# Kernel optimization log

Measured on AMD Instinct MI355X. Metric: run time of the kernel, lower is better.

Reference implementation:

```python
import jax, jax.numpy as jnp
import numpy as np

M, K, N = 32, 4096, 12288


def setup_inputs() -> dict:
    key = jax.random.key(0)
    k1, k2, k3, k4 = jax.random.split(key, 4)
    x = jax.random.normal(k1, (M, K), dtype=jnp.float32)
    # uint8-valued packed weight (stored as int32 for harness compatibility, values in [0,256))
    weight_u8 = jax.random.randint(k2, (K, N), 0, 256, dtype=jnp.int32)
    # per-output-channel fp16 scale and zero-point
    scale = (jax.random.uniform(k3, (N,), dtype=jnp.float32) * 0.01 + 1e-3).astype(jnp.float16)
    zero = (jax.random.uniform(k4, (N,), dtype=jnp.float32) * 255.0).astype(jnp.float16)
    return {"x": x, "weight_u8": weight_u8, "scale": scale, "zero": zero}


def reference(x, weight_u8, scale, zero):
    # QuantMatmulCustom: dequantize uint8 weight with per-channel fp16 scale/zero, then matmul.
    # w_deq[k, n] = (w_u8[k, n] - zero[n]) * scale[n]
    w_deq = (weight_u8.astype(jnp.float32) - zero.astype(jnp.float32)[None, :]) * scale.astype(jnp.float32)[None, :]
    # [M, K] @ [K, N] -> [M, N]
    return jnp.einsum('mk,kn->mn', x, w_deq)
```

## Files before the change

kernel.cpp:

```cpp
#include <hip/hip_runtime.h>

#define M_DIM 32
#define K_DIM 4096
#define N_DIM 12288
#define SPLITK 8
#define KPER  (K_DIM / SPLITK)
#define NT    (KPER / 32)
#define BLK   512
#define NPB   128

using bf16x8 = __attribute__((ext_vector_type(8))) short;
using f32x4  = __attribute__((ext_vector_type(4))) float;

typedef __attribute__((address_space(1))) const void GASV;
typedef __attribute__((address_space(3))) void LASV;

__device__ __forceinline__ short to_bf16(float f) {
    unsigned u = __float_as_uint(f);
    u += 0x7FFFu + ((u >> 16) & 1u);
    return (short)(u >> 16);
}

__device__ __forceinline__ bf16x8 pack_b(const int (&wv)[8]) {
    union { unsigned u[4]; bf16x8 v; } r;
    #pragma unroll
    for (int p = 0; p < 4; ++p) {
        unsigned a = __float_as_uint((float)wv[2 * p]);
        unsigned b = __float_as_uint((float)wv[2 * p + 1]);
        r.u[p] = __builtin_amdgcn_perm(b, a, 0x07060302);
    }
    return r.v;
}

__global__ __launch_bounds__(256) void qmm_prep(const float* __restrict__ x,
                                                short* __restrict__ frag,
                                                float* __restrict__ rowsum) {
    const int b   = blockIdx.x;
    const int tid = threadIdx.x;

    __shared__ float red[256];
    const float4* xr = (const float4*)(x + (size_t)b * K_DIM);
    float s = 0.f;
    #pragma unroll
    for (int i = 0; i < K_DIM / 4 / 256; ++i) {
        float4 v = xr[tid + 256 * i];
        s += v.x + v.y + v.z + v.w;
    }
    red[tid] = s;
    __syncthreads();
    #pragma unroll
    for (int off = 128; off > 0; off >>= 1) {
        if (tid < off) red[tid] += red[tid + off];
        __syncthreads();
    }
    if (tid == 0) rowsum[b] = red[0];

    #pragma unroll
    for (int i = 0; i < 2; ++i) {
        const int s2   = i * 256 + tid;
        const int kt   = 4 * b + (s2 >> 7);
        const int h    = (s2 >> 6) & 1;
        const int lane = s2 & 63;
        const int g    = lane >> 4;
        const int g0   = g & 1;
        const int m    = 16 * h + (lane & 15);
        const float* xp = x + (size_t)m * K_DIM + kt * 32 + 8 * g;
        float p0 = xp[0], p1 = xp[1], p2 = xp[2], p3 = xp[3];
        float p4 = xp[4], p5 = xp[5], p6 = xp[6], p7 = xp[7];
        bf16x8 v;
        v[0] = to_bf16(g0 ? p1 : p0);  v[1] = to_bf16(g0 ? p0 : p1);
        v[2] = to_bf16(g0 ? p3 : p2);  v[3] = to_bf16(g0 ? p2 : p3);
        v[4] = to_bf16(g0 ? p5 : p4);  v[5] = to_bf16(g0 ? p4 : p5);
        v[6] = to_bf16(g0 ? p7 : p6);  v[7] = to_bf16(g0 ? p6 : p7);
        *(bf16x8*)&frag[(size_t)((kt * 2 + h) * 64 + lane) * 8] = v;
    }
}

template <bool WS>
__global__ __launch_bounds__(BLK, 4) void qmm_main(const short* __restrict__ frag,
                                                   const int* __restrict__ w,
                                                   float* __restrict__ dst) {
    __shared__ int lds_b[8 * 2 * 512];

    const int tid  = threadIdx.x;
    const int lane = tid & 63;
    const int g    = lane >> 4;
    const int g0   = g & 1;
    const int c    = lane & 15;
    const int wid  = tid >> 6;
    const int k0   = blockIdx.y * KPER;
    const int n0w  = blockIdx.x * NPB + wid * 16;

    const int* gsrc[2];
    #pragma unroll
    for (int q = 0; q < 2; ++q)
        gsrc[q] = w + (size_t)(k0 + 16 * q + (lane >> 2)) * N_DIM + n0w + 4 * (lane & 3);

    int* const wbase = &lds_b[wid * 1024];

    const int vb = 4 * (128 * g + 4 * (c >> 2) + (c & 3));
    const int be = vb + 64 * g0;
    const int bo = vb + 64 * (1 - g0);

    const short* asrc = frag + ((size_t)(blockIdx.y * NT) * 1024 + lane * 8);

    f32x4 acc0 = {0.f, 0.f, 0.f, 0.f};
    f32x4 acc1 = {0.f, 0.f, 0.f, 0.f};
    bf16x8 aA0, aA1, aB0, aB1;

#define ISSUE(T) do {                                                            \
    __builtin_amdgcn_sched_barrier(0);                                           \
    __builtin_amdgcn_global_load_lds((GASV*)(gsrc[0] + (size_t)(32 * (T)) * N_DIM), \
        (LASV*)(wbase + ((T) & 1) * 512),       16, 0, 0);                       \
    __builtin_amdgcn_global_load_lds((GASV*)(gsrc[1] + (size_t)(32 * (T)) * N_DIM), \
        (LASV*)(wbase + ((T) & 1) * 512 + 256), 16, 0, 0);                       \
    if ((T) & 1) { aB0 = *(const bf16x8*)(asrc + (T) * 1024);                    \
                   aB1 = *(const bf16x8*)(asrc + (T) * 1024 + 512); }            \
    else         { aA0 = *(const bf16x8*)(asrc + (T) * 1024);                    \
                   aA1 = *(const bf16x8*)(asrc + (T) * 1024 + 512); }            \
    __builtin_amdgcn_sched_barrier(0);                                           \
} while (0)

#define WAITV(N) do { asm volatile("s_waitcnt vmcnt(" #N ")" ::: "memory");      \
    __builtin_amdgcn_sched_barrier(0); } while (0)

#define COMP(T) do {                                                             \
    char* pb = (char*)wbase + ((T) & 1) * 2048;                                  \
    int wv[8];                                                                   \
    wv[0] = *(int*)(pb + be);        wv[1] = *(int*)(pb + bo);                   \
    wv[2] = *(int*)(pb + be + 128);  wv[3] = *(int*)(pb + bo + 128);             \
    wv[4] = *(int*)(pb + be + 256);  wv[5] = *(int*)(pb + bo + 256);             \
    wv[6] = *(int*)(pb + be + 384);  wv[7] = *(int*)(pb + bo + 384);             \
    bf16x8 bfv = pack_b(wv);                                                     \
    acc0 = __builtin_amdgcn_mfma_f32_16x16x32_bf16(((T) & 1) ? aB0 : aA0, bfv, acc0, 0, 0, 0); \
    acc1 = __builtin_amdgcn_mfma_f32_16x16x32_bf16(((T) & 1) ? aB1 : aA1, bfv, acc1, 0, 0, 0); \
} while (0)

    ISSUE(0); ISSUE(1);
    WAITV(4); COMP(0);  ISSUE(2);
    WAITV(4); COMP(1);  ISSUE(3);
    WAITV(4); COMP(2);  ISSUE(4);
    WAITV(4); COMP(3);  ISSUE(5);
    WAITV(4); COMP(4);  ISSUE(6);
    WAITV(4); COMP(5);  ISSUE(7);
    WAITV(4); COMP(6);  ISSUE(8);
    WAITV(4); COMP(7);  ISSUE(9);
    WAITV(4); COMP(8);  ISSUE(10);
    WAITV(4); COMP(9);  ISSUE(11);
    WAITV(4); COMP(10); ISSUE(12);
    WAITV(4); COMP(11); ISSUE(13);
    WAITV(4); COMP(12); ISSUE(14);
    WAITV(4); COMP(13); ISSUE(15);
    WAITV(4); COMP(14);
    WAITV(0); COMP(15);

#undef ISSUE
#undef WAITV
#undef COMP

    if (WS) {
        float* pp = dst + ((size_t)blockIdx.y * M_DIM) * N_DIM + n0w + c;
        #pragma unroll
        for (int i = 0; i < 4; ++i) {
            const int r = 4 * (lane >> 4) + i;
            pp[(size_t)r * N_DIM]        = acc0[i];
            pp[(size_t)(16 + r) * N_DIM] = acc1[i];
        }
    } else {
        #pragma unroll
        for (int i = 0; i < 4; ++i) {
            const int r = 4 * (lane >> 4) + i;
            atomicAdd(&dst[(size_t)r * N_DIM + n0w + c], acc0[i]);
            atomicAdd(&dst[(size_t)(16 + r) * N_DIM + n0w + c], acc1[i]);
        }
    }
}

__global__ __launch_bounds__(256) void qmm_finalize(const float* __restrict__ part,
                                                    const float* __restrict__ rowsum,
                                                    const float* __restrict__ scale,
                                                    const float* __restrict__ zero,
                                                    float* __restrict__ out) {
    const int m  = blockIdx.y;
    const int n4 = blockIdx.x * 256 + threadIdx.x;
    const float rs = rowsum[m];
    float4 acc = make_float4(0.f, 0.f, 0.f, 0.f);
    #pragma unroll
    for (int sp = 0; sp < SPLITK; ++sp) {
        float4 p = ((const float4*)(part + ((size_t)sp * M_DIM + m) * N_DIM))[n4];
        acc.x += p.x; acc.y += p.y; acc.z += p.z; acc.w += p.w;
    }
    const float4 sc = ((const float4*)scale)[n4];
    const float4 zp = ((const float4*)zero)[n4];
    float4 o;
    o.x = sc.x * (acc.x - zp.x * rs);
    o.y = sc.y * (acc.y - zp.y * rs);
    o.z = sc.z * (acc.z - zp.z * rs);
    o.w = sc.w * (acc.w - zp.w * rs);
    ((float4*)(out + (size_t)m * N_DIM))[n4] = o;
}

__global__ __launch_bounds__(256) void qmm_zero(float* __restrict__ out) {
    int i = blockIdx.x * 256 + threadIdx.x;
    ((float4*)out)[i] = make_float4(0.f, 0.f, 0.f, 0.f);
}
__global__ __launch_bounds__(256) void qmm_scale(const float* __restrict__ x,
                                                 const float* __restrict__ scale,
                                                 const float* __restrict__ zero,
                                                 float* __restrict__ out) {
    const int m = blockIdx.y;
    __shared__ float red[256];
    float s = 0.f;
    for (int k = threadIdx.x; k < K_DIM; k += 256)
        s += x[(size_t)m * K_DIM + k];
    red[threadIdx.x] = s;
    __syncthreads();
    #pragma unroll
    for (int off = 128; off > 0; off >>= 1) {
        if (threadIdx.x < off) red[threadIdx.x] += red[threadIdx.x + off];
        __syncthreads();
    }
    const float rowsum = red[0];
    const int n = blockIdx.x * 256 + threadIdx.x;
    const float v = out[(size_t)m * N_DIM + n];
    out[(size_t)m * N_DIM + n] = scale[n] * (v - zero[n] * rowsum);
}

extern "C" void kernel_launch(void* const* d_in, const int* in_sizes, int n_in,
                              void* d_out, int out_size, void* d_ws, size_t ws_size,
                              hipStream_t stream) {
    const float* x     = (const float*)d_in[0];
    const int*   w     = (const int*)d_in[1];
    const float* scale = (const float*)d_in[2];
    const float* zero  = (const float*)d_in[3];
    float* out = (float*)d_out;

    const size_t frag_sz = (size_t)128 * 2 * 64 * 8 * sizeof(short);
    const size_t part_sz = (size_t)SPLITK * M_DIM * N_DIM * sizeof(float);
    short* fragp  = (short*)d_ws;
    float* rowsum = (float*)((char*)d_ws + frag_sz);
    float* part   = (float*)((char*)d_ws + frag_sz + 256);

    if (ws_size >= frag_sz + 256 + part_sz) {
        qmm_prep    <<<dim3(32),                 dim3(256), 0, stream>>>(x, fragp, rowsum);
        qmm_main<true><<<dim3(N_DIM / NPB, SPLITK), dim3(BLK), 0, stream>>>(fragp, w, part);
        qmm_finalize<<<dim3(N_DIM / 4 / 256, M_DIM), dim3(256), 0, stream>>>(part, rowsum, scale, zero, out);
    } else {
        qmm_prep    <<<dim3(32),                 dim3(256), 0, stream>>>(x, fragp, rowsum);
        qmm_zero    <<<dim3((M_DIM * N_DIM / 4) / 256), dim3(256), 0, stream>>>(out);
        qmm_main<false><<<dim3(N_DIM / NPB, SPLITK), dim3(BLK), 0, stream>>>(fragp, w, out);
        qmm_scale   <<<dim3(N_DIM / 256, M_DIM), dim3(256), 0, stream>>>(x, scale, zero, out);
    }
}
```

Before: 46.00 us.

## Fuse split-K reduction and dequant epilogue into main kernel via atomics

Drops the split-K partial buffer and the separate finalize kernel. The main kernel now applies the per-channel scale and the zero-point correction (only on the first K split) and atomically adds into the output. Zeroing of the output is folded into the prep kernel by enlarging its grid. This removes a kernel launch and the write and re-read of the 8-way partial buffer, at the cost of float atomics on the output, which makes the summation order nondeterministic. The fallback path is replaced by a simple non-MFMA kernel.

```diff
diff --git a/kernel.cpp b/kernel.cpp
--- a/kernel.cpp
+++ b/kernel.cpp
@@ -34,9 +34,14 @@
 
 __global__ __launch_bounds__(256) void qmm_prep(const float* __restrict__ x,
                                                 short* __restrict__ frag,
-                                                float* __restrict__ rowsum) {
-    const int b   = blockIdx.x;
+                                                float* __restrict__ rowsum,
+                                                float* __restrict__ out) {
     const int tid = threadIdx.x;
+    const int bid = blockIdx.x;
+
+    ((float4*)out)[bid * 256 + tid] = make_float4(0.f, 0.f, 0.f, 0.f);
+    if (bid >= 32) return;
+    const int b = bid;
 
     __shared__ float red[256];
     const float4* xr = (const float4*)(x + (size_t)b * K_DIM);
@@ -76,10 +81,12 @@
     }
 }
 
-template <bool WS>
 __global__ __launch_bounds__(BLK, 4) void qmm_main(const short* __restrict__ frag,
                                                    const int* __restrict__ w,
-                                                   float* __restrict__ dst) {
+                                                   const float* __restrict__ rowsum,
+                                                   const float* __restrict__ scale,
+                                                   const float* __restrict__ zero,
+                                                   float* __restrict__ out) {
     __shared__ int lds_b[8 * 2 * 512];
 
     const int tid  = threadIdx.x;
@@ -158,56 +165,57 @@
 #undef WAITV
 #undef COMP
 
-    if (WS) {
-        float* pp = dst + ((size_t)blockIdx.y * M_DIM) * N_DIM + n0w + c;
+    const float sc = scale[n0w + c];
+    float corr0[4] = {0.f, 0.f, 0.f, 0.f}, corr1[4] = {0.f, 0.f, 0.f, 0.f};
+    if (blockIdx.y == 0) {
+        const float zp = zero[n0w + c];
         #pragma unroll
         for (int i = 0; i < 4; ++i) {
             const int r = 4 * (lane >> 4) + i;
-            pp[(size_t)r * N_DIM]        = acc0[i];
-            pp[(size_t)(16 + r) * N_DIM] = acc1[i];
+            corr0[i] = zp * rowsum[r];
+            corr1[i] = zp * rowsum[16 + r];
         }
-    } else {
+    }
+    #pragma unroll
+    for (int i = 0; i < 4; ++i) {
+        const int r = 4 * (lane >> 4) + i;
+        atomicAdd(&out[(size_t)r * N_DIM + n0w + c],        sc * (acc0[i] - corr0[i]));
+        atomicAdd(&out[(size_t)(16 + r) * N_DIM + n0w + c], sc * (acc1[i] - corr1[i]));
+    }
+}
+
+__global__ __launch_bounds__(256) void qmm_zero_fb(float* __restrict__ out) {
+    int i = blockIdx.x * 256 + threadIdx.x;
+    ((float4*)out)[i] = make_float4(0.f, 0.f, 0.f, 0.f);
+}
+__global__ __launch_bounds__(256) void qmm_main_fb(const float* __restrict__ x,
+                                                   const int* __restrict__ w,
+                                                   float* __restrict__ out) {
+    const int n  = blockIdx.x * 256 + threadIdx.x;
+    const int k0 = blockIdx.y * 256;
+    float acc[M_DIM];
+    #pragma unroll
+    for (int m = 0; m < M_DIM; ++m) acc[m] = 0.f;
+    const int* wp = w + (size_t)k0 * N_DIM + n;
+    for (int kk = 0; kk < 256; kk += 4) {
+        const float w0 = (float)wp[(size_t)(kk + 0) * N_DIM];
+        const float w1 = (float)wp[(size_t)(kk + 1) * N_DIM];
+        const float w2 = (float)wp[(size_t)(kk + 2) * N_DIM];
+        const float w3 = (float)wp[(size_t)(kk + 3) * N_DIM];
         #pragma unroll
-        for (int i = 0; i < 4; ++i) {
-            const int r = 4 * (lane >> 4) + i;
-            atomicAdd(&dst[(size_t)r * N_DIM + n0w + c], acc0[i]);
-            atomicAdd(&dst[(size_t)(16 + r) * N_DIM + n0w + c], acc1[i]);
+        for (int m = 0; m < M_DIM; ++m) {
+            const float4 xv = *(const float4*)(x + (size_t)m * K_DIM + k0 + kk);
+            acc[m] = fmaf(xv.x, w0, fmaf(xv.y, w1, fmaf(xv.z, w2, fmaf(xv.w, w3, acc[m]))));
         }
     }
-}
-
-__global__ __launch_bounds__(256) void qmm_finalize(const float* __restrict__ part,
-                                                    const float* __restrict__ rowsum,
+    #pragma unroll
+    for (int m = 0; m < M_DIM; ++m)
+        atomicAdd(&out[(size_t)m * N_DIM + n], acc[m]);
+}
+__global__ __launch_bounds__(256) void qmm_scale_fb(const float* __restrict__ x,
                                                     const float* __restrict__ scale,
                                                     const float* __restrict__ zero,
                                                     float* __restrict__ out) {
-    const int m  = blockIdx.y;
-    const int n4 = blockIdx.x * 256 + threadIdx.x;
-    const float rs = rowsum[m];
-    float4 acc = make_float4(0.f, 0.f, 0.f, 0.f);
-    #pragma unroll
-    for (int sp = 0; sp < SPLITK; ++sp) {
-        float4 p = ((const float4*)(part + ((size_t)sp * M_DIM + m) * N_DIM))[n4];
-        acc.x += p.x; acc.y += p.y; acc.z += p.z; acc.w += p.w;
-    }
-    const float4 sc = ((const float4*)scale)[n4];
-    const float4 zp = ((const float4*)zero)[n4];
-    float4 o;
-    o.x = sc.x * (acc.x - zp.x * rs);
-    o.y = sc.y * (acc.y - zp.y * rs);
-    o.z = sc.z * (acc.z - zp.z * rs);
-    o.w = sc.w * (acc.w - zp.w * rs);
-    ((float4*)(out + (size_t)m * N_DIM))[n4] = o;
-}
-
-__global__ __launch_bounds__(256) void qmm_zero(float* __restrict__ out) {
-    int i = blockIdx.x * 256 + threadIdx.x;
-    ((float4*)out)[i] = make_float4(0.f, 0.f, 0.f, 0.f);
-}
-__global__ __launch_bounds__(256) void qmm_scale(const float* __restrict__ x,
-                                                 const float* __restrict__ scale,
-                                                 const float* __restrict__ zero,
-                                                 float* __restrict__ out) {
     const int m = blockIdx.y;
     __shared__ float red[256];
     float s = 0.f;
@@ -236,19 +244,15 @@
     float* out = (float*)d_out;
 
     const size_t frag_sz = (size_t)128 * 2 * 64 * 8 * sizeof(short);
-    const size_t part_sz = (size_t)SPLITK * M_DIM * N_DIM * sizeof(float);
     short* fragp  = (short*)d_ws;
     float* rowsum = (float*)((char*)d_ws + frag_sz);
-    float* part   = (float*)((char*)d_ws + frag_sz + 256);
-
-    if (ws_size >= frag_sz + 256 + part_sz) {
-        qmm_prep    <<<dim3(32),                 dim3(256), 0, stream>>>(x, fragp, rowsum);
-        qmm_main<true><<<dim3(N_DIM / NPB, SPLITK), dim3(BLK), 0, stream>>>(fragp, w, part);
-        qmm_finalize<<<dim3(N_DIM / 4 / 256, M_DIM), dim3(256), 0, stream>>>(part, rowsum, scale, zero, out);
+
+    if (ws_size >= frag_sz + 256) {
+        qmm_prep<<<dim3(M_DIM * N_DIM / 4 / 256), dim3(256), 0, stream>>>(x, fragp, rowsum, out);
+        qmm_main<<<dim3(N_DIM / NPB, SPLITK),     dim3(BLK), 0, stream>>>(fragp, w, rowsum, scale, zero, out);
     } else {
-        qmm_prep    <<<dim3(32),                 dim3(256), 0, stream>>>(x, fragp, rowsum);
-        qmm_zero    <<<dim3((M_DIM * N_DIM / 4) / 256), dim3(256), 0, stream>>>(out);
-        qmm_main<false><<<dim3(N_DIM / NPB, SPLITK), dim3(BLK), 0, stream>>>(fragp, w, out);
-        qmm_scale   <<<dim3(N_DIM / 256, M_DIM), dim3(256), 0, stream>>>(x, scale, zero, out);
-    }
-}
+        qmm_zero_fb <<<dim3(M_DIM * N_DIM / 4 / 256), dim3(256), 0, stream>>>(out);
+        qmm_main_fb <<<dim3(N_DIM / 256, 16),         dim3(256), 0, stream>>>(x, w, out);
+        qmm_scale_fb<<<dim3(N_DIM / 256, M_DIM),      dim3(256), 0, stream>>>(x, scale, zero, out);
+    }
+}
```

Result: faster. 43.17 us (-6.2%).
